# Performance work log

Measured on AMD Instinct MI355X. Metric: run time of the kernel, lower is better.

The kernel has to match this reference:

```python
import jax, jax.numpy as jnp
import numpy as np

# Constants from __init__ (domain bounds)
X_MIN, X_MAX = -1.0, 1.0
Y_MIN, Y_MAX = -1.0, 1.0
T_MIN, T_MAX = 0.0, 1.0

N_POINTS = 262144
WIDTH = 128
N_HIDDEN_STACK = 5  # hidden->hidden layers between first and last


def setup_inputs() -> dict:
    key = jax.random.key(0)
    ks = jax.random.split(key, 8)
    X = jax.random.uniform(ks[0], (N_POINTS, 4), dtype=jnp.float32)
    # glorot_normal-ish init
    def glorot(k, fan_in, fan_out, shape):
        std = (2.0 / (fan_in + fan_out)) ** 0.5
        return jax.random.normal(k, shape, dtype=jnp.float32) * std
    W0 = glorot(ks[1], 4, WIDTH, (4, WIDTH))
    b0 = jnp.zeros((WIDTH,), dtype=jnp.float32)
    Wh = glorot(ks[2], WIDTH, WIDTH, (N_HIDDEN_STACK, WIDTH, WIDTH))
    bh = jnp.zeros((N_HIDDEN_STACK, WIDTH), dtype=jnp.float32)
    WL = glorot(ks[3], WIDTH, 2, (WIDTH, 2))
    bL = jnp.zeros((2,), dtype=jnp.float32)
    nu_min = jnp.zeros((), dtype=jnp.float32)
    nu_max = jnp.ones((), dtype=jnp.float32)
    return {"X": X, "nu_min": nu_min, "nu_max": nu_max,
            "W0": W0, "b0": b0, "Wh": Wh, "bh": bh, "WL": WL, "bL": bL}


def _swish(x):
    return x * jax.nn.sigmoid(x)


def reference(X, nu_min, nu_max, W0, b0, Wh, bh, WL, bL):
    # Input rescaling to [-1, 1] per feature, then concat
    x_s = 2.0 * (X[:, 0:1] - X_MIN) / (X_MAX - X_MIN) - 1.0
    y_s = 2.0 * (X[:, 1:2] - Y_MIN) / (Y_MAX - Y_MIN) - 1.0
    t_s = 2.0 * (X[:, 2:3] - T_MIN) / (T_MAX - T_MIN) - 1.0
    nu_s = 2.0 * (X[:, 3:4] - nu_min) / (nu_max - nu_min) - 1.0
    H = jnp.concatenate([x_s, y_s, t_s, nu_s], axis=1)  # [N, 4]
    # Stacked small dense + swish layers (fused-MLP candidate)
    H = _swish(H @ W0 + b0)  # [N, WIDTH]
    for i in range(Wh.shape[0]):
        H = _swish(H @ Wh[i] + bh[i])
    return H @ WL + bL  # [N, 2], no activation on output layer
```

## Files before the change

### kernel.cpp

```cpp
#include <hip/hip_runtime.h>

typedef __bf16 bf16x8 __attribute__((ext_vector_type(8)));
typedef __bf16 bf16x2 __attribute__((ext_vector_type(2)));
typedef float  f32x4  __attribute__((ext_vector_type(4)));

#define WS_WT0_B 0
#define WS_WTH_B 8192
#define WS_WLT_B 172032

__device__ __forceinline__ unsigned short f2b(float f) {
  return __builtin_bit_cast(unsigned short, (__bf16)f);
}

__global__ void prep_kernel(const float* __restrict__ W0,
                            const float* __restrict__ Wh,
                            const float* __restrict__ WL,
                            unsigned short* __restrict__ ws) {
  int i = blockIdx.x * 256 + threadIdx.x;
  int l  = (i >> 3) & 63;
  int j  = i & 7;
  int lm = l & 15, lh = l >> 4;
  if (i < 4096) {
    int nt = i >> 9;
    int n = nt * 16 + lm, k = lh * 8 + j;
    ws[i] = f2b(k < 4 ? W0[k * 128 + n] : 0.f);
  } else if (i < 86016) {
    int t = i - 4096;
    int frag = t >> 9;
    int nt = frag & 7, ks = (frag >> 3) & 3, h = frag >> 5;
    int n = nt * 16 + lm, k = ks * 32 + lh * 8 + j;
    ws[i] = f2b(Wh[(h * 128 + k) * 128 + n]);
  } else if (i < 88064) {
    int t = i - 86016;
    int ks = t >> 9;
    int n = lm, k = ks * 32 + lh * 8 + j;
    ws[i] = f2b(n < 2 ? WL[k * 2 + n] : 0.f);
  }
}

__device__ __forceinline__ f32x4 swish4(f32x4 z) {
  f32x4 e;
  e[0] = __expf(-z[0]); e[1] = __expf(-z[1]);
  e[2] = __expf(-z[2]); e[3] = __expf(-z[3]);
  const f32x4 w = e + 1.f;
  f32x4 s;
  s[0] = __builtin_amdgcn_rcpf(w[0]); s[1] = __builtin_amdgcn_rcpf(w[1]);
  s[2] = __builtin_amdgcn_rcpf(w[2]); s[3] = __builtin_amdgcn_rcpf(w[3]);
  return z * s;
}

__device__ __forceinline__ uint2 pack4(f32x4 r) {
  bf16x2 lo = {(__bf16)r[0], (__bf16)r[1]};
  bf16x2 hi = {(__bf16)r[2], (__bf16)r[3]};
  uint2 wv;
  wv.x = __builtin_bit_cast(unsigned int, lo);
  wv.y = __builtin_bit_cast(unsigned int, hi);
  return wv;
}

__launch_bounds__(256, 4)
__global__ void mlp_kernel(const float* __restrict__ X,
                           const float* __restrict__ nu_min_p,
                           const float* __restrict__ nu_max_p,
                           const float* __restrict__ b0,
                           const float* __restrict__ bh,
                           const float* __restrict__ bL,
                           const unsigned short* __restrict__ ws,
                           float* __restrict__ out) {
  __shared__ __align__(16) char HsAll[4][32 * 256];
  const int lane = threadIdx.x & 63;
  const int wave = threadIdx.x >> 6;
  char* Hs = HsAll[wave];
  const int lm = lane & 15, lh = lane >> 4;
  const int row0 = blockIdx.x * 128 + wave * 32;
  const char* wsb = reinterpret_cast<const char*>(ws);
  const char* ap  = wsb + lane * 16;
  const int xorm = (lm & 7) << 4;

  const int va0 = lm * 256 + ((lh * 16) ^ xorm);
  const int va1 = va0 + 16 * 256;
  const int wa0 = lm * 256 + ((lh * 8) ^ xorm);
  const int wa1 = wa0 + 16 * 256;

  if (lane < 32) {
    const float4 xv = reinterpret_cast<const float4*>(X)[row0 + lane];
    const float numin = nu_min_p[0], numax = nu_max_p[0];
    const float v0 = xv.x;
    const float v1 = xv.y;
    const float v2 = 2.f * xv.z - 1.f;
    const float v3 = 2.f * (xv.w - numin) / (numax - numin) - 1.f;
    uint4 c0;
    c0.x = (unsigned)f2b(v0) | ((unsigned)f2b(v1) << 16);
    c0.y = (unsigned)f2b(v2) | ((unsigned)f2b(v3) << 16);
    c0.z = 0u; c0.w = 0u;
    const uint4 z4 = make_uint4(0u, 0u, 0u, 0u);
    const int xr = (lane & 7) << 4;
    char* rp = Hs + lane * 256;
    *reinterpret_cast<uint4*>(rp + (0  ^ xr)) = c0;
    *reinterpret_cast<uint4*>(rp + (16 ^ xr)) = z4;
    *reinterpret_cast<uint4*>(rp + (32 ^ xr)) = z4;
    *reinterpret_cast<uint4*>(rp + (48 ^ xr)) = z4;
  }

  f32x4 acc[8][2];

  {
    bf16x8 bfr[2];
    bfr[0] = __builtin_bit_cast(bf16x8, *reinterpret_cast<const uint4*>(Hs + va0));
    bfr[1] = __builtin_bit_cast(bf16x8, *reinterpret_cast<const uint4*>(Hs + va1));
#pragma unroll
    for (int nt = 0; nt < 8; ++nt) {
      const f32x4 bv = *reinterpret_cast<const f32x4*>(b0 + nt * 16 + lh * 4);
      const bf16x8 a = __builtin_bit_cast(bf16x8,
          *reinterpret_cast<const uint4*>(ap + WS_WT0_B + nt * 1024));
      acc[nt][0] = __builtin_amdgcn_mfma_f32_16x16x32_bf16(a, bfr[0], bv, 0, 0, 0);
      acc[nt][1] = __builtin_amdgcn_mfma_f32_16x16x32_bf16(a, bfr[1], bv, 0, 0, 0);
    }
#pragma unroll
    for (int nt = 0; nt < 8; ++nt) {
#pragma unroll
      for (int pt = 0; pt < 2; ++pt) {
        const uint2 wv = pack4(swish4(acc[nt][pt]));
        const int wa = (pt ? wa1 : wa0) ^ (nt << 5);
        *reinterpret_cast<uint2*>(Hs + wa) = wv;
      }
    }
  }

#pragma unroll
  for (int h = 0; h < 5; ++h) {
    const float* bias = bh + h * 128;
#pragma unroll
    for (int ks = 0; ks < 4; ++ks) {
      bf16x8 bfr[2];
      bfr[0] = __builtin_bit_cast(bf16x8,
          *reinterpret_cast<const uint4*>(Hs + (va0 ^ (ks << 6))));
      bfr[1] = __builtin_bit_cast(bf16x8,
          *reinterpret_cast<const uint4*>(Hs + (va1 ^ (ks << 6))));
#pragma unroll
      for (int nt = 0; nt < 8; ++nt) {
        const bf16x8 a = __builtin_bit_cast(bf16x8,
            *reinterpret_cast<const uint4*>(ap + WS_WTH_B + h * 32768 + (ks * 8 + nt) * 1024));
        if (ks == 0) {
          const f32x4 bv = *reinterpret_cast<const f32x4*>(bias + nt * 16 + lh * 4);
          acc[nt][0] = __builtin_amdgcn_mfma_f32_16x16x32_bf16(a, bfr[0], bv, 0, 0, 0);
          acc[nt][1] = __builtin_amdgcn_mfma_f32_16x16x32_bf16(a, bfr[1], bv, 0, 0, 0);
        } else {
          acc[nt][0] = __builtin_amdgcn_mfma_f32_16x16x32_bf16(a, bfr[0], acc[nt][0], 0, 0, 0);
          acc[nt][1] = __builtin_amdgcn_mfma_f32_16x16x32_bf16(a, bfr[1], acc[nt][1], 0, 0, 0);
        }
      }
    }
#pragma unroll
    for (int nt = 0; nt < 8; ++nt) {
#pragma unroll
      for (int pt = 0; pt < 2; ++pt) {
        const uint2 wv = pack4(swish4(acc[nt][pt]));
        const int wa = (pt ? wa1 : wa0) ^ (nt << 5);
        *reinterpret_cast<uint2*>(Hs + wa) = wv;
      }
    }
  }

  {
    const float bl0 = bL[0], bl1 = bL[1];
#pragma unroll
    for (int pt = 0; pt < 2; ++pt) {
      f32x4 accL = {0.f, 0.f, 0.f, 0.f};
#pragma unroll
      for (int ks = 0; ks < 4; ++ks) {
        const bf16x8 bfr = __builtin_bit_cast(bf16x8,
            *reinterpret_cast<const uint4*>(Hs + ((pt ? va1 : va0) ^ (ks << 6))));
        const bf16x8 a = __builtin_bit_cast(bf16x8,
            *reinterpret_cast<const uint4*>(ap + WS_WLT_B + ks * 1024));
        accL = __builtin_amdgcn_mfma_f32_16x16x32_bf16(a, bfr, accL, 0, 0, 0);
      }
      if (lh == 0) {
        const int p = pt * 16 + lm;
        float2 o;
        o.x = accL[0] + bl0;
        o.y = accL[1] + bl1;
        *reinterpret_cast<float2*>(out + (size_t)(row0 + p) * 2) = o;
      }
    }
  }
}

extern "C" void kernel_launch(void* const* d_in, const int* in_sizes, int n_in,
                              void* d_out, int out_size, void* d_ws, size_t ws_size,
                              hipStream_t stream) {
  const float* X     = (const float*)d_in[0];
  const float* numin = (const float*)d_in[1];
  const float* numax = (const float*)d_in[2];
  const float* W0    = (const float*)d_in[3];
  const float* b0    = (const float*)d_in[4];
  const float* Wh    = (const float*)d_in[5];
  const float* bh    = (const float*)d_in[6];
  const float* WL    = (const float*)d_in[7];
  const float* bL    = (const float*)d_in[8];
  unsigned short* ws = (unsigned short*)d_ws;
  float* out = (float*)d_out;

  hipLaunchKernelGGL(prep_kernel, dim3(344), dim3(256), 0, stream, W0, Wh, WL, ws);
  hipLaunchKernelGGL(mlp_kernel, dim3(2048), dim3(256), 0, stream,
                     X, numin, numax, b0, bh, bL, ws, out);
}
```

Before: 87.91 us.

## Use single-wave blocks with double-buffered weight fragment prefetch across K-steps

Blocks shrink to one wavefront of 32 rows (8192 blocks) instead of four waves per block. The hidden-layer loop is restructured so weight fragments for the next K-step, and the next layer or output layer, are loaded from global memory into two register sets while the current MFMAs run, with sched barriers enforcing the ordering. Biases are staged in LDS and added after accumulation instead of seeding the accumulator. The WL fragment region is padded so the final prefetch stays in bounds. This aims to hide global weight-load latency, at the cost of more VGPRs and possibly lower occupancy, since __launch_bounds__ is now (64, 2).

```diff
diff --git a/kernel.cpp b/kernel.cpp
--- a/kernel.cpp
+++ b/kernel.cpp
@@ -30,11 +30,11 @@
     int nt = frag & 7, ks = (frag >> 3) & 3, h = frag >> 5;
     int n = nt * 16 + lm, k = ks * 32 + lh * 8 + j;
     ws[i] = f2b(Wh[(h * 128 + k) * 128 + n]);
-  } else if (i < 88064) {
+  } else if (i < 90112) {
     int t = i - 86016;
-    int ks = t >> 9;
-    int n = lm, k = ks * 32 + lh * 8 + j;
-    ws[i] = f2b(n < 2 ? WL[k * 2 + n] : 0.f);
+    int f = t >> 9;
+    int k = (f & 3) * 32 + lh * 8 + j;
+    ws[i] = f2b((f < 4 && lm < 2) ? WL[k * 2 + lm] : 0.f);
   }
 }
 
@@ -58,7 +58,12 @@
   return wv;
 }
 
-__launch_bounds__(256, 4)
+#define SB() __builtin_amdgcn_sched_barrier(0)
+#define GLD(addr) __builtin_bit_cast(bf16x8, *reinterpret_cast<const uint4*>(addr))
+#define LRD(addr) __builtin_bit_cast(bf16x8, *reinterpret_cast<const uint4*>(addr))
+#define MFMA(a, b, c) __builtin_amdgcn_mfma_f32_16x16x32_bf16((a), (b), (c), 0, 0, 0)
+
+__launch_bounds__(64, 2)
 __global__ void mlp_kernel(const float* __restrict__ X,
                            const float* __restrict__ nu_min_p,
                            const float* __restrict__ nu_max_p,
@@ -67,20 +72,29 @@
                            const float* __restrict__ bL,
                            const unsigned short* __restrict__ ws,
                            float* __restrict__ out) {
-  __shared__ __align__(16) char HsAll[4][32 * 256];
-  const int lane = threadIdx.x & 63;
-  const int wave = threadIdx.x >> 6;
-  char* Hs = HsAll[wave];
+  __shared__ __align__(16) char smem[32 * 256 + 5 * 128 * 4];
+  char* Hs = smem;
+  float* bias_lds = reinterpret_cast<float*>(smem + 8192);
+  const int lane = threadIdx.x;
   const int lm = lane & 15, lh = lane >> 4;
-  const int row0 = blockIdx.x * 128 + wave * 32;
-  const char* wsb = reinterpret_cast<const char*>(ws);
-  const char* ap  = wsb + lane * 16;
+  const int row0 = blockIdx.x * 32;
+  const char* ap = reinterpret_cast<const char*>(ws) + lane * 16;
   const int xorm = (lm & 7) << 4;
-
   const int va0 = lm * 256 + ((lh * 16) ^ xorm);
   const int va1 = va0 + 16 * 256;
   const int wa0 = lm * 256 + ((lh * 8) ^ xorm);
   const int wa1 = wa0 + 16 * 256;
+
+  bf16x8 aL0[8];
+#pragma unroll
+  for (int nt = 0; nt < 8; ++nt) aL0[nt] = GLD(ap + WS_WT0_B + nt * 1024);
+  f32x4 bv0[8];
+#pragma unroll
+  for (int nt = 0; nt < 8; ++nt)
+    bv0[nt] = *reinterpret_cast<const f32x4*>(b0 + nt * 16 + lh * 4);
+  float bstg[10];
+#pragma unroll
+  for (int i = 0; i < 10; ++i) bstg[i] = bh[i * 64 + lane];
 
   if (lane < 32) {
     const float4 xv = reinterpret_cast<const float4*>(X)[row0 + lane];
@@ -101,63 +115,85 @@
     *reinterpret_cast<uint4*>(rp + (32 ^ xr)) = z4;
     *reinterpret_cast<uint4*>(rp + (48 ^ xr)) = z4;
   }
+#pragma unroll
+  for (int i = 0; i < 10; ++i) bias_lds[i * 64 + lane] = bstg[i];
 
   f32x4 acc[8][2];
-
-  {
-    bf16x8 bfr[2];
-    bfr[0] = __builtin_bit_cast(bf16x8, *reinterpret_cast<const uint4*>(Hs + va0));
-    bfr[1] = __builtin_bit_cast(bf16x8, *reinterpret_cast<const uint4*>(Hs + va1));
-#pragma unroll
-    for (int nt = 0; nt < 8; ++nt) {
-      const f32x4 bv = *reinterpret_cast<const f32x4*>(b0 + nt * 16 + lh * 4);
-      const bf16x8 a = __builtin_bit_cast(bf16x8,
-          *reinterpret_cast<const uint4*>(ap + WS_WT0_B + nt * 1024));
-      acc[nt][0] = __builtin_amdgcn_mfma_f32_16x16x32_bf16(a, bfr[0], bv, 0, 0, 0);
-      acc[nt][1] = __builtin_amdgcn_mfma_f32_16x16x32_bf16(a, bfr[1], bv, 0, 0, 0);
-    }
-#pragma unroll
-    for (int nt = 0; nt < 8; ++nt) {
+  bf16x8 bfrA[2], bfrB[2];
+  bf16x8 aA[8], aB[8];
+
+  bfrA[0] = LRD(Hs + va0);
+  bfrA[1] = LRD(Hs + va1);
+#pragma unroll
+  for (int nt = 0; nt < 8; ++nt) {
+    acc[nt][0] = MFMA(aL0[nt], bfrA[0], bv0[nt]);
+    acc[nt][1] = MFMA(aL0[nt], bfrA[1], bv0[nt]);
+  }
+#pragma unroll
+  for (int nt = 0; nt < 8; ++nt) aA[nt] = GLD(ap + WS_WTH_B + nt * 1024);
+#pragma unroll
+  for (int nt = 0; nt < 8; ++nt) {
+#pragma unroll
+    for (int pt = 0; pt < 2; ++pt) {
+      const uint2 wv = pack4(swish4(acc[nt][pt]));
+      *reinterpret_cast<uint2*>(Hs + ((pt ? wa1 : wa0) ^ (nt << 5))) = wv;
+    }
+  }
+
+  const f32x4 zero4 = {0.f, 0.f, 0.f, 0.f};
+
+#pragma unroll 1
+  for (int h = 0; h < 5; ++h) {
+    const char* wb = ap + WS_WTH_B + h * 32768;
+    const float* bl = bias_lds + h * 128;
+
+    bfrA[0] = LRD(Hs + va0);
+    bfrA[1] = LRD(Hs + va1);
+#pragma unroll
+    for (int nt = 0; nt < 8; ++nt) aB[nt] = GLD(wb + 8192 + nt * 1024);
+    bfrB[0] = LRD(Hs + (va0 ^ 64));
+    bfrB[1] = LRD(Hs + (va1 ^ 64));
+#pragma unroll
+    for (int nt = 0; nt < 8; ++nt) {
+      acc[nt][0] = MFMA(aA[nt], bfrA[0], zero4);
+      acc[nt][1] = MFMA(aA[nt], bfrA[1], zero4);
+    }
+    SB();
+#pragma unroll
+    for (int nt = 0; nt < 8; ++nt) aA[nt] = GLD(wb + 16384 + nt * 1024);
+    bfrA[0] = LRD(Hs + (va0 ^ 128));
+    bfrA[1] = LRD(Hs + (va1 ^ 128));
+#pragma unroll
+    for (int nt = 0; nt < 8; ++nt) {
+      acc[nt][0] = MFMA(aB[nt], bfrB[0], acc[nt][0]);
+      acc[nt][1] = MFMA(aB[nt], bfrB[1], acc[nt][1]);
+    }
+    SB();
+#pragma unroll
+    for (int nt = 0; nt < 8; ++nt) aB[nt] = GLD(wb + 24576 + nt * 1024);
+    bfrB[0] = LRD(Hs + (va0 ^ 192));
+    bfrB[1] = LRD(Hs + (va1 ^ 192));
+#pragma unroll
+    for (int nt = 0; nt < 8; ++nt) {
+      acc[nt][0] = MFMA(aA[nt], bfrA[0], acc[nt][0]);
+      acc[nt][1] = MFMA(aA[nt], bfrA[1], acc[nt][1]);
+    }
+    SB();
+#pragma unroll
+    for (int nt = 0; nt < 8; ++nt) aA[nt] = GLD(wb + 32768 + nt * 1024);
+#pragma unroll
+    for (int nt = 0; nt < 8; ++nt) {
+      acc[nt][0] = MFMA(aB[nt], bfrB[0], acc[nt][0]);
+      acc[nt][1] = MFMA(aB[nt], bfrB[1], acc[nt][1]);
+    }
+    SB();
+#pragma unroll
+    for (int nt = 0; nt < 8; ++nt) {
+      const f32x4 bv = *reinterpret_cast<const f32x4*>(bl + nt * 16 + lh * 4);
 #pragma unroll
       for (int pt = 0; pt < 2; ++pt) {
-        const uint2 wv = pack4(swish4(acc[nt][pt]));
-        const int wa = (pt ? wa1 : wa0) ^ (nt << 5);
-        *reinterpret_cast<uint2*>(Hs + wa) = wv;
-      }
-    }
-  }
-
-#pragma unroll
-  for (int h = 0; h < 5; ++h) {
-    const float* bias = bh + h * 128;
-#pragma unroll
-    for (int ks = 0; ks < 4; ++ks) {
-      bf16x8 bfr[2];
-      bfr[0] = __builtin_bit_cast(bf16x8,
-          *reinterpret_cast<const uint4*>(Hs + (va0 ^ (ks << 6))));
-      bfr[1] = __builtin_bit_cast(bf16x8,
-          *reinterpret_cast<const uint4*>(Hs + (va1 ^ (ks << 6))));
-#pragma unroll
-      for (int nt = 0; nt < 8; ++nt) {
-        const bf16x8 a = __builtin_bit_cast(bf16x8,
-            *reinterpret_cast<const uint4*>(ap + WS_WTH_B + h * 32768 + (ks * 8 + nt) * 1024));
-        if (ks == 0) {
-          const f32x4 bv = *reinterpret_cast<const f32x4*>(bias + nt * 16 + lh * 4);
-          acc[nt][0] = __builtin_amdgcn_mfma_f32_16x16x32_bf16(a, bfr[0], bv, 0, 0, 0);
-          acc[nt][1] = __builtin_amdgcn_mfma_f32_16x16x32_bf16(a, bfr[1], bv, 0, 0, 0);
-        } else {
-          acc[nt][0] = __builtin_amdgcn_mfma_f32_16x16x32_bf16(a, bfr[0], acc[nt][0], 0, 0, 0);
-          acc[nt][1] = __builtin_amdgcn_mfma_f32_16x16x32_bf16(a, bfr[1], acc[nt][1], 0, 0, 0);
-        }
-      }
-    }
-#pragma unroll
-    for (int nt = 0; nt < 8; ++nt) {
-#pragma unroll
-      for (int pt = 0; pt < 2; ++pt) {
-        const uint2 wv = pack4(swish4(acc[nt][pt]));
-        const int wa = (pt ? wa1 : wa0) ^ (nt << 5);
-        *reinterpret_cast<uint2*>(Hs + wa) = wv;
+        const uint2 wv = pack4(swish4(acc[nt][pt] + bv));
+        *reinterpret_cast<uint2*>(Hs + ((pt ? wa1 : wa0) ^ (nt << 5))) = wv;
       }
     }
   }
@@ -169,11 +205,8 @@
       f32x4 accL = {0.f, 0.f, 0.f, 0.f};
 #pragma unroll
       for (int ks = 0; ks < 4; ++ks) {
-        const bf16x8 bfr = __builtin_bit_cast(bf16x8,
-            *reinterpret_cast<const uint4*>(Hs + ((pt ? va1 : va0) ^ (ks << 6))));
-        const bf16x8 a = __builtin_bit_cast(bf16x8,
-            *reinterpret_cast<const uint4*>(ap + WS_WLT_B + ks * 1024));
-        accL = __builtin_amdgcn_mfma_f32_16x16x32_bf16(a, bfr, accL, 0, 0, 0);
+        const bf16x8 bfr = LRD(Hs + ((pt ? va1 : va0) ^ (ks << 6)));
+        accL = MFMA(aA[ks], bfr, accL);
       }
       if (lh == 0) {
         const int p = pt * 16 + lm;
@@ -201,7 +234,7 @@
   unsigned short* ws = (unsigned short*)d_ws;
   float* out = (float*)d_out;
 
-  hipLaunchKernelGGL(prep_kernel, dim3(344), dim3(256), 0, stream, W0, Wh, WL, ws);
-  hipLaunchKernelGGL(mlp_kernel, dim3(2048), dim3(256), 0, stream,
+  hipLaunchKernelGGL(prep_kernel, dim3(352), dim3(256), 0, stream, W0, Wh, WL, ws);
+  hipLaunchKernelGGL(mlp_kernel, dim3(8192), dim3(64), 0, stream,
                      X, numin, numax, b0, bh, bL, ws, out);
 }
```

After: 78.26 us. -11.0%, faster.
